# Kernel optimization log

Measured on AMD Instinct MI355X. Metric: run time of the kernel, lower is better.

## Reference

```python
import jax, jax.numpy as jnp
import numpy as np

B, DIM = 16384, 1024
H1, H2, H3 = 500, 200, 200


def setup_inputs() -> dict:
    key = jax.random.key(0)
    ks = jax.random.split(key, 16)
    s = 0.01
    return {
        "x": jax.random.normal(ks[0], (B, DIM), dtype=jnp.float32),
        "show_index": jax.random.randint(ks[1], (B,), 0, 100),
        "st": jax.random.normal(ks[2], (1000, 16), dtype=jnp.float32),
        # deep MLP params (shared across the two task heads, as in the source)
        "W1": jax.random.normal(ks[3], (DIM, H1), dtype=jnp.float32) * s,
        "b1": jnp.zeros((H1,), dtype=jnp.float32),
        "W2": jax.random.normal(ks[4], (H1, H2), dtype=jnp.float32) * s,
        "b2": jnp.zeros((H2,), dtype=jnp.float32),
        "W3": jax.random.normal(ks[5], (H2, H3), dtype=jnp.float32) * s,
        "b3": jnp.zeros((H3,), dtype=jnp.float32),
        # final sigmoid head on concat([emb(DIM), d3(H3)])
        "Wl": jax.random.normal(ks[6], (DIM + H3, 1), dtype=jnp.float32) * s,
        "bl": jnp.zeros((1,), dtype=jnp.float32),
        # per-(task, cross-layer) cross weights/biases: tf.random_normal stddev=0.01
        "cw": jax.random.normal(ks[7], (2, 3, DIM), dtype=jnp.float32) * s,
        "cb": jax.random.normal(ks[8], (2, 3, DIM), dtype=jnp.float32) * s,
    }


def reference(x, show_index, st, W1, b1, W2, b2, W3, b3, Wl, bl, cw, cb):
    # Deep part (same shared Dense layers each task -> compute once).
    d = jax.nn.relu(x @ W1 + b1)
    d = jax.nn.relu(d @ W2 + b2)
    d3 = jax.nn.relu(d @ W3 + b3)  # (B, H3)

    # cross_net: sum_i w[j] * x[b,i] * emb[b,j]  ==  x.sum(1) * emb[b,j] * w[j]
    # (collapsed form of the (B,dim,dim) outer product + axis-1 reduction)
    xsum = jnp.sum(x, axis=1, keepdims=True)  # (B, 1)
    preds = []
    for i in range(2):
        emb = x
        for j in range(3):
            emb = xsum * emb * cw[i, j] + cb[i, j] + x
        mid = jnp.concatenate([emb, d3], axis=-1)  # (B, DIM+H3)
        preds.append(jax.nn.sigmoid(mid @ Wl + bl))  # (B, 1)
    return tuple(preds)
```

## Files before the change

kernel.cpp:

```cpp
#include <hip/hip_runtime.h>
#include <hip/hip_bf16.h>
#include <math.h>

#define B_ROWS 16384
#define DIM 1024

typedef __attribute__((ext_vector_type(8))) short s16x8;
typedef __attribute__((ext_vector_type(4))) float f32x4;

static __device__ __forceinline__ unsigned short f2bf(float f) {
    union { float f; unsigned u; } v; v.f = f;
    unsigned r = v.u + 0x7FFF + ((v.u >> 16) & 1);
    return (unsigned short)(r >> 16);
}

static __device__ __forceinline__ unsigned cvt_pk_bf16(float lo, float hi) {
    unsigned r;
    asm volatile("v_cvt_pk_bf16_f32 %0, %1, %2" : "=v"(r) : "v"(lo), "v"(hi));
    return r;
}

static __device__ __forceinline__ void gload16(const unsigned short* g, unsigned short* l) {
    __builtin_amdgcn_global_load_lds(
        (const __attribute__((address_space(1))) unsigned int*)g,
        (__attribute__((address_space(3))) unsigned int*)l, 16, 0, 0);
}

__global__ __launch_bounds__(256) void prep(
    const float* __restrict__ W1, const float* __restrict__ W2,
    const float* __restrict__ W3,
    const float* __restrict__ cw, const float* __restrict__ cb,
    const float* __restrict__ Wl,
    unsigned short* __restrict__ W1b, unsigned short* __restrict__ W2b,
    unsigned short* __restrict__ W3b,
    float* __restrict__ czz) {
    __shared__ unsigned short tile[64][72];
    __shared__ float red[4][6];
    const int tid = threadIdx.x;
    const int blk = blockIdx.x;

    if (blk < 176) {
        const int w = blk;
        const float* src; unsigned short* dst;
        int kt, nt, Ksrc, Nsrc, ldDst;
        bool skipHi = false;
        if (w < 128)      { kt = w & 15;         nt = w >> 4;         src = W1; dst = W1b; Ksrc = 1024; Nsrc = 500; ldDst = 1024; skipHi = true; }
        else if (w < 160) { kt = (w - 128) & 7;  nt = (w - 128) >> 3; src = W2; dst = W2b; Ksrc = 500;  Nsrc = 200; ldDst = 512;  }
        else              { kt = (w - 160) & 3;  nt = (w - 160) >> 2; src = W3; dst = W3b; Ksrc = 200;  Nsrc = 200; ldDst = 256;  }
        const int k0 = kt << 6, n0 = nt << 6;
        {
            const int r = tid >> 2, c0 = (tid & 3) << 4;
            const int kk = k0 + r;
#pragma unroll
            for (int i = 0; i < 16; ++i) {
                const int nn = n0 + c0 + i;
                const float v = (kk < Ksrc && nn < Nsrc) ? src[(size_t)kk * Nsrc + nn] : 0.f;
                tile[r][c0 + i] = f2bf(v);
            }
        }
        __syncthreads();
        {
            const int n = tid >> 2, kc = (tid & 3) << 4;
            if (!(skipHi && (n0 + n) >= 500)) {
                unsigned short* o = dst + (size_t)(n0 + n) * ldDst + k0 + kc;
#pragma unroll
                for (int i = 0; i < 16; ++i) o[i] = tile[kc + i][n];
            }
        }
    } else if (blk == 176) {
#pragma unroll
        for (int q = 0; q < 4; ++q) {
            const int k = tid * 4 + q;
            const float wl = Wl[k];
            const float a1 = cw[k],         a2 = cw[1024 + k],  a3 = cw[2048 + k];
            const float d1_ = cw[3072 + k], d2_ = cw[4096 + k], d3_ = cw[5120 + k];
            W1b[(size_t)500 * 1024 + k] = f2bf(a1 * a2 * a3 * wl);
            W1b[(size_t)501 * 1024 + k] = f2bf(a2 * a3 * wl);
            W1b[(size_t)502 * 1024 + k] = f2bf(a3 * wl);
            W1b[(size_t)503 * 1024 + k] = f2bf(d1_ * d2_ * d3_ * wl);
            W1b[(size_t)504 * 1024 + k] = f2bf(d2_ * d3_ * wl);
            W1b[(size_t)505 * 1024 + k] = f2bf(d3_ * wl);
            W1b[(size_t)506 * 1024 + k] = f2bf(wl);
            W1b[(size_t)507 * 1024 + k] = 0x3F80;
            W1b[(size_t)508 * 1024 + k] = 0;
            W1b[(size_t)509 * 1024 + k] = 0;
            W1b[(size_t)510 * 1024 + k] = 0;
            W1b[(size_t)511 * 1024 + k] = 0;
        }
    } else {
        float c[6] = {0.f, 0.f, 0.f, 0.f, 0.f, 0.f};
#pragma unroll
        for (int q = 0; q < 4; ++q) {
            const int k = tid * 4 + q;
            const float wl = Wl[k];
            {
                const float w2 = cw[1024 + k], w3 = cw[2048 + k];
                const float b1 = cb[k], b2 = cb[1024 + k], b3 = cb[2048 + k];
                c[0] += w2 * w3 * b1 * wl;
                c[1] += w3 * b2 * wl;
                c[2] += b3 * wl;
            }
            {
                const float w2 = cw[4096 + k], w3 = cw[5120 + k];
                const float b1 = cb[3072 + k], b2 = cb[4096 + k], b3 = cb[5120 + k];
                c[3] += w2 * w3 * b1 * wl;
                c[4] += w3 * b2 * wl;
                c[5] += b3 * wl;
            }
        }
        const int lane = tid & 63, wv = tid >> 6;
#pragma unroll
        for (int j = 0; j < 6; ++j)
#pragma unroll
            for (int m = 1; m < 64; m <<= 1) c[j] += __shfl_xor(c[j], m, 64);
        if (lane == 0)
#pragma unroll
            for (int j = 0; j < 6; ++j) red[wv][j] = c[j];
        __syncthreads();
        if (tid < 6) czz[tid] = red[0][tid] + red[1][tid] + red[2][tid] + red[3][tid];
    }
}

template <int ROWS>
static __device__ __forceinline__ void stage8(
    const unsigned short* __restrict__ src, int K, int rowBase, int kt,
    unsigned short* lds, int w, int lane) {
    const int r8   = lane >> 3;
    const int slot = lane & 7;
#pragma unroll
    for (int q = 0; q < ROWS / 64; ++q) {
        const int blk   = q * 8 + w;
        const int row   = blk * 8 + r8;
        const int chunk = slot ^ (row & 7);
        const unsigned short* g = src + (size_t)(rowBase + row) * K + kt * 64 + chunk * 8;
        gload16(g, lds + blk * 512);
    }
}

__global__ __launch_bounds__(512, 4) void gemm_xa(
    const float* __restrict__ X,
    const unsigned short* __restrict__ Bw,
    const float* __restrict__ bias,
    unsigned short* __restrict__ C,
    float* __restrict__ zparts) {
    constexpr int K = 1024, ldc = 512, nK = 16;
    __shared__ unsigned short As[2][128 * 64];
    __shared__ unsigned short Bs[2][128 * 64];

    const int tid  = threadIdx.x;
    const int lane = tid & 63;
    const int wid  = tid >> 6;
    const int wm   = wid >> 2;
    const int wn   = wid & 3;
    const int g    = lane >> 4;
    const int r16  = lane & 15;

    const int cpx = gridDim.x >> 3;
    const int swz = (blockIdx.x & 7) * cpx + (blockIdx.x >> 3);
    const int rowBase = (swz >> 2) << 7;
    const int colBase = (swz & 3) << 7;

    const int arow = tid >> 2;
    const int ak   = (tid & 3) << 4;
    const float* aSrc = X + (size_t)(rowBase + arow) * K + ak;

    float4 a_regs[4];

    f32x4 acc[4][2];
#pragma unroll
    for (int m = 0; m < 4; ++m)
#pragma unroll
        for (int n = 0; n < 2; ++n)
            acc[m][n] = (f32x4){0.f, 0.f, 0.f, 0.f};

    auto issue_A = [&](int kt) {
#pragma unroll
        for (int q = 0; q < 4; ++q)
            a_regs[q] = *(const float4*)(aSrc + kt * 64 + q * 4);
    };
    auto cvt_write_A = [&](unsigned short* dst) {
        const int cb = (tid & 3) << 1;
        uint4 v0, v1;
        v0.x = cvt_pk_bf16(a_regs[0].x, a_regs[0].y);
        v0.y = cvt_pk_bf16(a_regs[0].z, a_regs[0].w);
        v0.z = cvt_pk_bf16(a_regs[1].x, a_regs[1].y);
        v0.w = cvt_pk_bf16(a_regs[1].z, a_regs[1].w);
        v1.x = cvt_pk_bf16(a_regs[2].x, a_regs[2].y);
        v1.y = cvt_pk_bf16(a_regs[2].z, a_regs[2].w);
        v1.z = cvt_pk_bf16(a_regs[3].x, a_regs[3].y);
        v1.w = cvt_pk_bf16(a_regs[3].z, a_regs[3].w);
        const int ch0 = (cb + 0) ^ (arow & 7);
        const int ch1 = (cb + 1) ^ (arow & 7);
        *(uint4*)((char*)dst + arow * 128 + ch0 * 16) = v0;
        *(uint4*)((char*)dst + arow * 128 + ch1 * 16) = v1;
    };

    issue_A(0);
    asm volatile("" ::: "memory");
    stage8<128>(Bw, K, colBase, 0, Bs[0], wid, lane);
    asm volatile("" ::: "memory");
    cvt_write_A(As[0]);
    asm volatile("s_waitcnt vmcnt(0)" ::: "memory");
    asm volatile("s_waitcnt lgkmcnt(0)" ::: "memory");
    __builtin_amdgcn_s_barrier();
    asm volatile("" ::: "memory");

    for (int kt = 0; kt < nK; ++kt) {
        const int buf = kt & 1;
        if (kt + 1 < nK) {
            issue_A(kt + 1);
            asm volatile("" ::: "memory");
            stage8<128>(Bw, K, colBase, kt + 1, Bs[buf ^ 1], wid, lane);
            asm volatile("" ::: "memory");
        }

        const unsigned short* Ab = As[buf];
        const unsigned short* Bb = Bs[buf];
#pragma unroll
        for (int ks = 0; ks < 2; ++ks) {
            s16x8 af[4], bfr[2];
#pragma unroll
            for (int m = 0; m < 4; ++m) {
                const int row = wm * 64 + m * 16 + r16;
                const int off = ((ks * 4 + g) * 16) ^ ((row & 7) << 4);
                af[m] = *(const s16x8*)((const char*)Ab + row * 128 + off);
            }
#pragma unroll
            for (int n = 0; n < 2; ++n) {
                const int row = wn * 32 + n * 16 + r16;
                const int off = ((ks * 4 + g) * 16) ^ ((row & 7) << 4);
                bfr[n] = *(const s16x8*)((const char*)Bb + row * 128 + off);
            }
#pragma unroll
            for (int m = 0; m < 4; ++m)
#pragma unroll
                for (int n = 0; n < 2; ++n)
                    acc[m][n] = __builtin_amdgcn_mfma_f32_16x16x32_bf16(af[m], bfr[n], acc[m][n], 0, 0, 0);
        }

        if (kt + 1 < nK) {
            cvt_write_A(As[buf ^ 1]);
        }
        asm volatile("s_waitcnt vmcnt(0)" ::: "memory");
        asm volatile("s_waitcnt lgkmcnt(0)" ::: "memory");
        __builtin_amdgcn_s_barrier();
        asm volatile("" ::: "memory");
    }

    unsigned short* Cb = As[0];
#pragma unroll
    for (int n = 0; n < 2; ++n) {
        const int lcol = wn * 32 + n * 16 + r16;
        const int col = colBase + lcol;
        const float bv = (col < 500) ? bias[col] : 0.f;
        const unsigned pc = (unsigned)(col - 500);
#pragma unroll
        for (int m = 0; m < 4; ++m) {
            const int lrow = wm * 64 + m * 16 + g * 4;
#pragma unroll
            for (int r = 0; r < 4; ++r) {
                const float raw = acc[m][n][r];
                if (pc < 8u) zparts[(size_t)(rowBase + lrow + r) * 8 + pc] = raw;
                float v = raw + bv;
                v = v > 0.f ? v : 0.f;
                Cb[(lrow + r) * 128 + lcol] = f2bf(v);
            }
        }
    }
    __syncthreads();

    {
        const int row = tid >> 2;
        const int q   = tid & 3;
        const uint4* s = (const uint4*)(Cb + row * 128 + q * 32);
        uint4* d = (uint4*)(C + (size_t)(rowBase + row) * ldc + colBase + q * 32);
        d[0] = s[0];
        d[1] = s[1];
    }
}

__global__ __launch_bounds__(512) void tail_fused(
    const unsigned short* __restrict__ d1,
    const unsigned short* __restrict__ W2b,
    const float* __restrict__ b2,
    const unsigned short* __restrict__ W3b,
    const float* __restrict__ b3,
    const float* __restrict__ Wl,
    const float* __restrict__ bl,
    const float* __restrict__ zparts,
    const float* __restrict__ czz,
    float* __restrict__ out) {
    __shared__ unsigned short As[2][64 * 64];
    __shared__ unsigned short Bs[2][256 * 64];
    __shared__ unsigned short P[64 * 256];
    __shared__ float part[8][64];

    const int tid  = threadIdx.x;
    const int lane = tid & 63;
    const int wid  = tid >> 6;
    const int wm   = wid >> 2;
    const int wn   = wid & 3;
    const int g    = lane >> 4;
    const int r16  = lane & 15;
    const int rowBase = blockIdx.x << 6;

    f32x4 acc[2][4];
#pragma unroll
    for (int m = 0; m < 2; ++m)
#pragma unroll
        for (int n = 0; n < 4; ++n)
            acc[m][n] = (f32x4){0.f, 0.f, 0.f, 0.f};

    stage8<64>(d1, 512, rowBase, 0, As[0], wid, lane);
    stage8<256>(W2b, 512, 0, 0, Bs[0], wid, lane);

    for (int kt = 0; kt < 8; ++kt) {
        const int buf = kt & 1;
        if (kt + 1 < 8) {
            stage8<64>(d1, 512, rowBase, kt + 1, As[buf ^ 1], wid, lane);
            stage8<256>(W2b, 512, 0, kt + 1, Bs[buf ^ 1], wid, lane);
            asm volatile("s_waitcnt vmcnt(5)" ::: "memory");
        } else {
            asm volatile("s_waitcnt vmcnt(0)" ::: "memory");
        }
        __builtin_amdgcn_s_barrier();
        asm volatile("" ::: "memory");

        const unsigned short* Ab = As[buf];
        const unsigned short* Bb = Bs[buf];
#pragma unroll
        for (int ks = 0; ks < 2; ++ks) {
            s16x8 af[2], bfr[4];
#pragma unroll
            for (int m = 0; m < 2; ++m) {
                const int row = wm * 32 + m * 16 + r16;
                const int off = ((ks * 4 + g) * 16) ^ ((row & 7) << 4);
                af[m] = *(const s16x8*)((const char*)Ab + row * 128 + off);
            }
#pragma unroll
            for (int n = 0; n < 4; ++n) {
                const int row = wn * 64 + n * 16 + r16;
                const int off = ((ks * 4 + g) * 16) ^ ((row & 7) << 4);
                bfr[n] = *(const s16x8*)((const char*)Bb + row * 128 + off);
            }
#pragma unroll
            for (int m = 0; m < 2; ++m)
#pragma unroll
                for (int n = 0; n < 4; ++n)
                    acc[m][n] = __builtin_amdgcn_mfma_f32_16x16x32_bf16(af[m], bfr[n], acc[m][n], 0, 0, 0);
        }
        asm volatile("s_waitcnt lgkmcnt(0)" ::: "memory");
        __builtin_amdgcn_s_barrier();
        asm volatile("" ::: "memory");
    }

#pragma unroll
    for (int n = 0; n < 4; ++n) {
        const int col = wn * 64 + n * 16 + r16;
        const float bv = (col < 200) ? b2[col] : 0.f;
#pragma unroll
        for (int m = 0; m < 2; ++m) {
#pragma unroll
            for (int r = 0; r < 4; ++r) {
                const int row = wm * 32 + m * 16 + g * 4 + r;
                float v = acc[m][n][r] + bv;
                v = v > 0.f ? v : 0.f;
                const int byte = row * 512 + ((col * 2) ^ ((row & 7) << 4));
                *(unsigned short*)((char*)P + byte) = f2bf(v);
            }
        }
    }

    stage8<256>(W3b, 256, 0, 0, Bs[0], wid, lane);
    asm volatile("s_waitcnt lgkmcnt(0)" ::: "memory");
    __builtin_amdgcn_s_barrier();
    asm volatile("" ::: "memory");

    f32x4 acc2[2][4];
#pragma unroll
    for (int m = 0; m < 2; ++m)
#pragma unroll
        for (int n = 0; n < 4; ++n)
            acc2[m][n] = (f32x4){0.f, 0.f, 0.f, 0.f};

    for (int kt = 0; kt < 4; ++kt) {
        const int buf = kt & 1;
        if (kt + 1 < 4) {
            stage8<256>(W3b, 256, 0, kt + 1, Bs[buf ^ 1], wid, lane);
            asm volatile("s_waitcnt vmcnt(4)" ::: "memory");
        } else {
            asm volatile("s_waitcnt vmcnt(0)" ::: "memory");
        }
        __builtin_amdgcn_s_barrier();
        asm volatile("" ::: "memory");

        const unsigned short* Bb = Bs[buf];
#pragma unroll
        for (int ks = 0; ks < 2; ++ks) {
            s16x8 af[2], bfr[4];
#pragma unroll
            for (int m = 0; m < 2; ++m) {
                const int row = wm * 32 + m * 16 + r16;
                const int byte = row * 512 + ((kt * 128 + (ks * 4 + g) * 16) ^ ((row & 7) << 4));
                af[m] = *(const s16x8*)((const char*)P + byte);
            }
#pragma unroll
            for (int n = 0; n < 4; ++n) {
                const int row = wn * 64 + n * 16 + r16;
                const int off = ((ks * 4 + g) * 16) ^ ((row & 7) << 4);
                bfr[n] = *(const s16x8*)((const char*)Bb + row * 128 + off);
            }
#pragma unroll
            for (int m = 0; m < 2; ++m)
#pragma unroll
                for (int n = 0; n < 4; ++n)
                    acc2[m][n] = __builtin_amdgcn_mfma_f32_16x16x32_bf16(af[m], bfr[n], acc2[m][n], 0, 0, 0);
        }
        asm volatile("s_waitcnt lgkmcnt(0)" ::: "memory");
        __builtin_amdgcn_s_barrier();
        asm volatile("" ::: "memory");
    }

    float wlv[4], b3v[4];
#pragma unroll
    for (int n = 0; n < 4; ++n) {
        const int col = wn * 64 + n * 16 + r16;
        wlv[n] = (col < 200) ? Wl[1024 + col] : 0.f;
        b3v[n] = (col < 200) ? b3[col] : 0.f;
    }
#pragma unroll
    for (int m = 0; m < 2; ++m) {
#pragma unroll
        for (int r = 0; r < 4; ++r) {
            float s = 0.f;
#pragma unroll
            for (int n = 0; n < 4; ++n) {
                float v = acc2[m][n][r] + b3v[n];
                v = v > 0.f ? v : 0.f;
                s += v * wlv[n];
            }
            s += __shfl_xor(s, 1, 64);
            s += __shfl_xor(s, 2, 64);
            s += __shfl_xor(s, 4, 64);
            s += __shfl_xor(s, 8, 64);
            if (r16 == 0) part[wid][wm * 32 + m * 16 + g * 4 + r] = s;
        }
    }
    __syncthreads();

    if (tid < 64) {
        const int row = rowBase + tid;
        const int wmr = (tid >> 5) << 2;
        const float t = part[wmr][tid] + part[wmr + 1][tid] +
                        part[wmr + 2][tid] + part[wmr + 3][tid];
        const float blv = bl[0];
        const float* zp = zparts + (size_t)row * 8;
        float4 zpa = *(const float4*)(zp);
        float4 zpb = *(const float4*)(zp + 4);
        const float s = zpb.w;
        const float z0 = ((zpa.x * s + zpa.y + czz[0]) * s + zpa.z + czz[1]) * s
                         + zpb.z + czz[2] + t + blv;
        const float z1 = ((zpa.w * s + zpb.x + czz[3]) * s + zpb.y + czz[4]) * s
                         + zpb.z + czz[5] + t + blv;
        out[row]          = 1.f / (1.f + expf(-z0));
        out[B_ROWS + row] = 1.f / (1.f + expf(-z1));
    }
}

extern "C" void kernel_launch(void* const* d_in, const int* in_sizes, int n_in,
                              void* d_out, int out_size, void* d_ws, size_t ws_size,
                              hipStream_t stream) {
    const float* x  = (const float*)d_in[0];
    const float* W1 = (const float*)d_in[3];
    const float* b1 = (const float*)d_in[4];
    const float* W2 = (const float*)d_in[5];
    const float* b2 = (const float*)d_in[6];
    const float* W3 = (const float*)d_in[7];
    const float* b3 = (const float*)d_in[8];
    const float* Wl = (const float*)d_in[9];
    const float* bl = (const float*)d_in[10];
    const float* cw = (const float*)d_in[11];
    const float* cb = (const float*)d_in[12];
    float* out = (float*)d_out;

    unsigned short* d1  = (unsigned short*)d_ws;
    unsigned short* W1b = d1 + (size_t)16384 * 512;
    unsigned short* W2b = W1b + (size_t)512 * 1024;
    unsigned short* W3b = W2b + (size_t)256 * 512;
    float* zparts = (float*)(W3b + (size_t)256 * 256);
    float* czz = zparts + (size_t)16384 * 8;

    prep<<<178, 256, 0, stream>>>(W1, W2, W3, cw, cb, Wl, W1b, W2b, W3b, czz);

    gemm_xa<<<512, 512, 0, stream>>>(x, W1b, b1, d1, zparts);

    tail_fused<<<256, 512, 0, stream>>>(d1, W2b, b2, W3b, b3, Wl, bl,
                                        zparts, czz, out);
}
```

Baseline: 55.31 us.

## Deepen gemm_xa prefetch to two stages with register double-bank and triple B buffer

Prefetches A (fp32 into two register banks) and B (via global_load_lds into a triple LDS buffer) two k-tiles ahead instead of one. Waits use partial vmcnt counts so the newest tile's loads can stay in flight across the barrier. This is meant to hide more global load latency in the first GEMM. It costs extra registers and LDS (a third B buffer), which may lower occupancy under launch_bounds(512,4), and it depends on the vmcnt counts matching the number of issued loads exactly.

```diff
diff --git a/kernel.cpp b/kernel.cpp
--- a/kernel.cpp
+++ b/kernel.cpp
@@ -145,7 +145,7 @@
     float* __restrict__ zparts) {
     constexpr int K = 1024, ldc = 512, nK = 16;
     __shared__ unsigned short As[2][128 * 64];
-    __shared__ unsigned short Bs[2][128 * 64];
+    __shared__ unsigned short Bs[3][128 * 64];
 
     const int tid  = threadIdx.x;
     const int lane = tid & 63;
@@ -161,10 +161,9 @@
     const int colBase = (swz & 3) << 7;
 
     const int arow = tid >> 2;
-    const int ak   = (tid & 3) << 4;
-    const float* aSrc = X + (size_t)(rowBase + arow) * K + ak;
-
-    float4 a_regs[4];
+    const float* aSrc = X + (size_t)(rowBase + arow) * K + ((tid & 3) << 4);
+
+    float4 bank0[4], bank1[4];
 
     f32x4 acc[4][2];
 #pragma unroll
@@ -173,49 +172,56 @@
         for (int n = 0; n < 2; ++n)
             acc[m][n] = (f32x4){0.f, 0.f, 0.f, 0.f};
 
-    auto issue_A = [&](int kt) {
-#pragma unroll
-        for (int q = 0; q < 4; ++q)
-            a_regs[q] = *(const float4*)(aSrc + kt * 64 + q * 4);
-    };
-    auto cvt_write_A = [&](unsigned short* dst) {
-        const int cb = (tid & 3) << 1;
-        uint4 v0, v1;
-        v0.x = cvt_pk_bf16(a_regs[0].x, a_regs[0].y);
-        v0.y = cvt_pk_bf16(a_regs[0].z, a_regs[0].w);
-        v0.z = cvt_pk_bf16(a_regs[1].x, a_regs[1].y);
-        v0.w = cvt_pk_bf16(a_regs[1].z, a_regs[1].w);
-        v1.x = cvt_pk_bf16(a_regs[2].x, a_regs[2].y);
-        v1.y = cvt_pk_bf16(a_regs[2].z, a_regs[2].w);
-        v1.z = cvt_pk_bf16(a_regs[3].x, a_regs[3].y);
-        v1.w = cvt_pk_bf16(a_regs[3].z, a_regs[3].w);
-        const int ch0 = (cb + 0) ^ (arow & 7);
-        const int ch1 = (cb + 1) ^ (arow & 7);
-        *(uint4*)((char*)dst + arow * 128 + ch0 * 16) = v0;
-        *(uint4*)((char*)dst + arow * 128 + ch1 * 16) = v1;
-    };
-
-    issue_A(0);
+#define ISSUE_A(kt_, bank_)                                                   \
+    {                                                                         \
+        _Pragma("unroll")                                                     \
+        for (int q = 0; q < 4; ++q)                                           \
+            bank_[q] = *(const float4*)(aSrc + (kt_) * 64 + q * 4);           \
+    }
+
+#define CVT_WRITE_A(bank_, dst_)                                              \
+    {                                                                         \
+        const int cb_ = (tid & 3) << 1;                                       \
+        uint4 v0_, v1_;                                                       \
+        v0_.x = cvt_pk_bf16(bank_[0].x, bank_[0].y);                          \
+        v0_.y = cvt_pk_bf16(bank_[0].z, bank_[0].w);                          \
+        v0_.z = cvt_pk_bf16(bank_[1].x, bank_[1].y);                          \
+        v0_.w = cvt_pk_bf16(bank_[1].z, bank_[1].w);                          \
+        v1_.x = cvt_pk_bf16(bank_[2].x, bank_[2].y);                          \
+        v1_.y = cvt_pk_bf16(bank_[2].z, bank_[2].w);                          \
+        v1_.z = cvt_pk_bf16(bank_[3].x, bank_[3].y);                          \
+        v1_.w = cvt_pk_bf16(bank_[3].z, bank_[3].w);                          \
+        const int ch0_ = (cb_ + 0) ^ (arow & 7);                              \
+        const int ch1_ = (cb_ + 1) ^ (arow & 7);                              \
+        *(uint4*)((char*)(dst_) + arow * 128 + ch0_ * 16) = v0_;              \
+        *(uint4*)((char*)(dst_) + arow * 128 + ch1_ * 16) = v1_;              \
+    }
+
+    ISSUE_A(0, bank0);
+    asm volatile("" ::: "memory");
+    ISSUE_A(1, bank1);
     asm volatile("" ::: "memory");
     stage8<128>(Bw, K, colBase, 0, Bs[0], wid, lane);
+    stage8<128>(Bw, K, colBase, 1, Bs[1], wid, lane);
     asm volatile("" ::: "memory");
-    cvt_write_A(As[0]);
-    asm volatile("s_waitcnt vmcnt(0)" ::: "memory");
+    CVT_WRITE_A(bank0, As[0]);
+    asm volatile("s_waitcnt vmcnt(2)" ::: "memory");
     asm volatile("s_waitcnt lgkmcnt(0)" ::: "memory");
     __builtin_amdgcn_s_barrier();
     asm volatile("" ::: "memory");
 
     for (int kt = 0; kt < nK; ++kt) {
-        const int buf = kt & 1;
-        if (kt + 1 < nK) {
-            issue_A(kt + 1);
+        const unsigned short* Ab = As[kt & 1];
+        const unsigned short* Bb = Bs[kt % 3];
+
+        if (kt + 2 < nK) {
+            if ((kt & 1) == 0) { ISSUE_A(kt + 2, bank0); }
+            else               { ISSUE_A(kt + 2, bank1); }
             asm volatile("" ::: "memory");
-            stage8<128>(Bw, K, colBase, kt + 1, Bs[buf ^ 1], wid, lane);
+            stage8<128>(Bw, K, colBase, kt + 2, Bs[(kt + 2) % 3], wid, lane);
             asm volatile("" ::: "memory");
         }
 
-        const unsigned short* Ab = As[buf];
-        const unsigned short* Bb = Bs[buf];
 #pragma unroll
         for (int ks = 0; ks < 2; ++ks) {
             s16x8 af[4], bfr[2];
@@ -239,13 +245,20 @@
         }
 
         if (kt + 1 < nK) {
-            cvt_write_A(As[buf ^ 1]);
-        }
-        asm volatile("s_waitcnt vmcnt(0)" ::: "memory");
+            if ((kt & 1) == 0) { CVT_WRITE_A(bank1, As[1]); }
+            else               { CVT_WRITE_A(bank0, As[0]); }
+        }
+
+        if (kt + 2 < nK)
+            asm volatile("s_waitcnt vmcnt(6)" ::: "memory");
+        else
+            asm volatile("s_waitcnt vmcnt(0)" ::: "memory");
         asm volatile("s_waitcnt lgkmcnt(0)" ::: "memory");
         __builtin_amdgcn_s_barrier();
         asm volatile("" ::: "memory");
     }
+#undef ISSUE_A
+#undef CVT_WRITE_A
 
     unsigned short* Cb = As[0];
 #pragma unroll
```

Measured after the change: 55.56 us. No clear change (+0.5%).
